# Performance work log

Measured on AMD Instinct MI355X. Metric: run time of the kernel, lower is better.

## Reference

```python
import jax, jax.numpy as jnp
import numpy as np

B, S, D, H = 1, 2048, 1024, 16
DH = D // H  # 64
HID = 4 * D
EPS = 1e-5
NEG = -1.0e9


def setup_inputs() -> dict:
    key = jax.random.key(0)
    ks = jax.random.split(key, 12)
    s = 0.02
    return {
        "y": jax.random.normal(ks[0], (B, S, D), jnp.float32),
        "encoder_output": jax.random.normal(ks[1], (B, S, D), jnp.float32),
        # per-head shared projection (query_fc used for q,k,v — faithful to source bug)
        "Wq_self": jax.random.normal(ks[2], (H, D, DH), jnp.float32) * s,
        "bq_self": jax.random.normal(ks[3], (H, DH), jnp.float32) * s,
        "Wq_cross": jax.random.normal(ks[4], (H, D, DH), jnp.float32) * s,
        "bq_cross": jax.random.normal(ks[5], (H, DH), jnp.float32) * s,
        "g1": jnp.ones((D,), jnp.float32), "beta1": jnp.zeros((D,), jnp.float32),
        "g2": jnp.ones((D,), jnp.float32), "beta2": jnp.zeros((D,), jnp.float32),
        "g3": jnp.ones((D,), jnp.float32), "beta3": jnp.zeros((D,), jnp.float32),
        "w1": jax.random.normal(ks[6], (D, HID), jnp.float32) * s,
        "b1": jax.random.normal(ks[7], (HID,), jnp.float32) * s,
        "w2": jax.random.normal(ks[8], (HID, D), jnp.float32) * s,
        "b2": jax.random.normal(ks[9], (D,), jnp.float32) * s,
    }


def _layernorm(x, g, b):
    mu = jnp.mean(x, axis=-1, keepdims=True)
    var = jnp.mean((x - mu) ** 2, axis=-1, keepdims=True)
    return (x - mu) * jax.lax.rsqrt(var + EPS) * g + b


def _mha(x_q, x_kv, W, bias, causal):
    # source bug: q, k, v all use query_fc projection
    q = jnp.einsum('bsd,hde->bhse', x_q, W) + bias[None, :, None, :]
    k = jnp.einsum('bsd,hde->bhse', x_kv, W) + bias[None, :, None, :]
    v = jnp.einsum('bsd,hde->bhse', x_kv, W) + bias[None, :, None, :]
    scores = jnp.einsum('bhse,bhte->bhst', q, k) / jnp.sqrt(jnp.float32(DH))
    if causal:
        sq, sk = scores.shape[-2], scores.shape[-1]
        mask = jnp.triu(jnp.ones((sq, sk), bool), k=1)
        scores = jnp.where(mask, NEG, scores)
    p = jax.nn.softmax(scores, axis=-1)
    out = jnp.einsum('bhst,bhte->bhse', p, v)  # [B,H,S,DH]
    b, h, s, e = out.shape
    return out.transpose(0, 2, 1, 3).reshape(b, s, h * e)


def reference(y, encoder_output, Wq_self, bq_self, Wq_cross, bq_cross,
              g1, beta1, g2, beta2, g3, beta3, w1, b1, w2, b2):
    sa = _mha(y, y, Wq_self, bq_self, causal=True)
    y1 = _layernorm(y + sa, g1, beta1)
    ca = _mha(y1, encoder_output, Wq_cross, bq_cross, causal=False)
    y2 = _layernorm(y1 + ca, g2, beta2)
    ff = jnp.maximum(y2 @ w1 + b1, 0.0) @ w2 + b2
    return _layernorm(y2 + ff, g3, beta3)
```

## Files before the change

kernel.cpp:

```cpp
#include <hip/hip_runtime.h>
#include <hip/hip_bf16.h>


#define S_LEN 2048
#define DMODEL 1024
#define NHEAD 16
#define DHEAD 64
#define HIDDEN 4096

using bf16 = __hip_bfloat16;
typedef __attribute__((ext_vector_type(8))) short bf16x8;
typedef __attribute__((ext_vector_type(4))) float floatx4;

__device__ __forceinline__ void async_ld16(const void* g, void* l) {
  __builtin_amdgcn_global_load_lds(
      (const __attribute__((address_space(1))) unsigned int*)g,
      (__attribute__((address_space(3))) unsigned int*)l, 16, 0, 0);
}

__device__ __forceinline__ unsigned short f2bf_bits(float f) {
  __hip_bfloat16 b = __float2bfloat16(f);
  return *(unsigned short*)&b;
}

template <bool HEADB>
__global__ __launch_bounds__(256) void transp_bf16_kernel(
    const float* __restrict__ src0, bf16* __restrict__ dst0,
    const float* __restrict__ src1, bf16* __restrict__ dst1, int K, int N) {
  const float* src = blockIdx.z ? src1 : src0;
  bf16* dst = blockIdx.z ? dst1 : dst0;
  __shared__ float tile[32][33];
  const int tx = threadIdx.x & 31, ty = threadIdx.x >> 5;
  const int k0 = blockIdx.y * 32, n0 = blockIdx.x * 32;
#pragma unroll
  for (int i = 0; i < 4; ++i) {
    const int k = k0 + ty + i * 8;
    const int n = n0 + tx;
    size_t idx;
    if (HEADB)
      idx = (size_t)(n >> 6) * ((size_t)K * 64) + (size_t)k * 64 + (n & 63);
    else
      idx = (size_t)k * N + n;
    tile[ty + i * 8][tx] = src[idx];
  }
  __syncthreads();
#pragma unroll
  for (int i = 0; i < 4; ++i) {
    const int n = n0 + ty + i * 8;
    const int k = k0 + tx;
    dst[(size_t)n * K + k] = __float2bfloat16(tile[tx][ty + i * 8]);
  }
}

__global__ __launch_bounds__(256) void conv_bf16_kernel(
    const float* __restrict__ src0, bf16* __restrict__ dst0,
    const float* __restrict__ src1, bf16* __restrict__ dst1, int n4) {
  const float* src = blockIdx.z ? src1 : src0;
  bf16* dst = blockIdx.z ? dst1 : dst0;
  const int i = blockIdx.x * 256 + threadIdx.x;
  if (i >= n4) return;
  float4 v = ((const float4*)src)[i];
  unsigned short r[4] = {f2bf_bits(v.x), f2bf_bits(v.y), f2bf_bits(v.z), f2bf_bits(v.w)};
  ((ushort2*)dst)[i * 2] = make_ushort2(r[0], r[1]);
  ((ushort2*)dst)[i * 2 + 1] = make_ushort2(r[2], r[3]);
}

template <int BM, int BN, bool RELU, bool DUALT, typename CT>
__global__ __launch_bounds__(256) void mfma_gemm_kernel(
    const bf16* __restrict__ A0, const bf16* __restrict__ Bt0,
    const float* __restrict__ bias0, CT* __restrict__ C0,
    bf16* __restrict__ Ct0,
    const bf16* __restrict__ A1, const bf16* __restrict__ Bt1,
    const float* __restrict__ bias1, CT* __restrict__ C1,
    bf16* __restrict__ Ct1,
    int M, int N, int Kstride, int Klen) {
  const bf16* A = blockIdx.z ? A1 : A0;
  const bf16* Bt = blockIdx.z ? Bt1 : Bt0;
  const float* bias = blockIdx.z ? bias1 : bias0;
  CT* C = blockIdx.z ? C1 : C0;
  bf16* Ct = blockIdx.z ? Ct1 : Ct0;

  constexpr int MF = (BM + 31) / 32;
  constexpr int NF = BN / 32;
  __shared__ __align__(16) bf16 As[2][BM * 64];
  __shared__ __align__(16) bf16 Bs[2][BN * 64];

  const int tid = threadIdx.x;
  const int wave = tid >> 6;
  const int lane = tid & 63;
  const int m0 = blockIdx.y * BM;
  const int n0 = blockIdx.x * BN;
  const int wr = wave >> 1, wc = wave & 1;

  const int srow = tid >> 3;
  const int schunk = (tid & 7) ^ (srow & 7);
  const bf16* agp = A + (size_t)(m0 + srow) * Kstride + schunk * 8;
  const bf16* bgp = Bt + (size_t)(n0 + srow) * Kstride + schunk * 8;

  floatx4 acc[MF][NF];
#pragma unroll
  for (int i = 0; i < MF; ++i)
#pragma unroll
    for (int j = 0; j < NF; ++j) acc[i][j] = floatx4{0.f, 0.f, 0.f, 0.f};

  const int mrow = lane & 15;
  const int p0 = (((lane >> 4) ^ (mrow & 7)) << 4);
  const int p1 = p0 ^ 64;

  auto stage = [&](int buf, int kt) {
    char* al = (char*)As + buf * (BM * 128) + wave * 1024;
    char* bl = (char*)Bs + buf * (BN * 128) + wave * 1024;
#pragma unroll
    for (int i = 0; i < BM / 32; ++i)
      async_ld16(agp + (size_t)(32 * i) * Kstride + kt, al + i * 4096);
#pragma unroll
    for (int i = 0; i < BN / 32; ++i)
      async_ld16(bgp + (size_t)(32 * i) * Kstride + kt, bl + i * 4096);
  };

  stage(0, 0);
  __syncthreads();

  int cur = 0;
  for (int kt = 0; kt < Klen; kt += 64) {
    const char* abase = (const char*)As + cur * (BM * 128);
    const char* bbase = (const char*)Bs + cur * (BN * 128);
    bf16x8 af0[MF], af1[MF], bf0[NF], bf1[NF];
#pragma unroll
    for (int fi = 0; fi < MF; ++fi) {
      const char* ar = abase + (wr * (BM / 2) + fi * 16 + mrow) * 128;
      af0[fi] = *(const bf16x8*)(ar + p0);
      af1[fi] = *(const bf16x8*)(ar + p1);
    }
#pragma unroll
    for (int fj = 0; fj < NF; ++fj) {
      const char* br = bbase + (wc * (BN / 2) + fj * 16 + mrow) * 128;
      bf0[fj] = *(const bf16x8*)(br + p0);
      bf1[fj] = *(const bf16x8*)(br + p1);
    }

    if (kt + 64 < Klen) stage(cur ^ 1, kt + 64);

#pragma unroll
    for (int fi = 0; fi < MF; ++fi)
#pragma unroll
      for (int fj = 0; fj < NF; ++fj) {
        acc[fi][fj] = __builtin_amdgcn_mfma_f32_16x16x32_bf16(
            af0[fi], bf0[fj], acc[fi][fj], 0, 0, 0);
        acc[fi][fj] = __builtin_amdgcn_mfma_f32_16x16x32_bf16(
            af1[fi], bf1[fj], acc[fi][fj], 0, 0, 0);
      }

    __syncthreads();
    cur ^= 1;
  }

  const int erow = (lane >> 4) * 4;
  const int ecol = lane & 15;
#pragma unroll
  for (int fi = 0; fi < MF; ++fi) {
#pragma unroll
    for (int fj = 0; fj < NF; ++fj) {
      const int nn = n0 + wc * (BN / 2) + fj * 16 + ecol;
      const float bv = bias ? bias[nn] : 0.0f;
      const int mmb = m0 + wr * (BM / 2) + fi * 16 + erow;
      float v[4];
#pragma unroll
      for (int r = 0; r < 4; ++r) {
        v[r] = acc[fi][fj][r] + bv;
        if (RELU) v[r] = fmaxf(v[r], 0.0f);
        if constexpr (sizeof(CT) == 2)
          C[(size_t)(mmb + r) * N + nn] = (CT)__float2bfloat16(v[r]);
        else
          C[(size_t)(mmb + r) * N + nn] = (CT)v[r];
      }
      if (DUALT) {
        ushort4 pk;
        pk.x = f2bf_bits(v[0]);
        pk.y = f2bf_bits(v[1]);
        pk.z = f2bf_bits(v[2]);
        pk.w = f2bf_bits(v[3]);
        *(ushort4*)&Ct[(size_t)nn * M + mmb] = pk;
      }
    }
  }
}

__global__ __launch_bounds__(256) void mfma_attn_kernel(
    const bf16* __restrict__ Q, const bf16* __restrict__ K,
    const bf16* __restrict__ Vt,
    float* __restrict__ OA, float* __restrict__ OB,
    float* __restrict__ LA, float* __restrict__ LB, int causal) {
  __shared__ __align__(16) unsigned short Kt[2][32 * 64];
  __shared__ __align__(16) unsigned short Vs[2][64 * 32];
  __shared__ __align__(16) unsigned short Ps[4][512];

  const int tid = threadIdx.x;
  const int w = tid >> 6, lane = tid & 63;
  const int g = lane >> 4, c = lane & 15;
  const int h = blockIdx.y;
  const int qb = causal ? ((int)gridDim.x - 1 - (int)blockIdx.x)
                        : (int)blockIdx.x;
  const int q0 = qb * 64;
  const int z = blockIdx.z;
  const int qw = q0 + w * 16;
  float* Oz = z ? OB : OA;
  float* Lz = z ? LB : LA;

  const bf16* qrow = Q + (size_t)(qw + c) * DMODEL + h * DHEAD + g * 8;
  const bf16x8 qfa = *(const bf16x8*)qrow;
  const bf16x8 qfb = *(const bf16x8*)(qrow + 32);

  const int srk = tid >> 3;
  const int sck = (tid & 7) ^ (srk & 7);
  const bf16* kgp = K + (size_t)srk * DMODEL + h * DHEAD + sck * 8;
  const int srv = tid >> 2;
  const int scv = (tid & 3) ^ ((srv >> 1) & 3);
  const bf16* vgp = Vt + (size_t)(h * DHEAD + srv) * S_LEN + scv * 8;

  const int kpos0 = ((g ^ (c & 7)) << 4);
  const int kpos1 = kpos0 ^ 64;
  const int vpos = ((g ^ ((c >> 1) & 3)) << 4);
  char* pswave = (char*)Ps + w * 1024;

  floatx4 of[4];
#pragma unroll
  for (int md = 0; md < 4; ++md) of[md] = floatx4{0.f, 0.f, 0.f, 0.f};
  float lpart = 0.f;

  const int nkt = causal ? (q0 / 32 + 2) : (S_LEN / 32);

  auto stage = [&](int buf, int kt) {
    const int t0 = kt * 32;
    async_ld16(kgp + (size_t)t0 * DMODEL, (char*)Kt + buf * 4096 + w * 1024);
    async_ld16(vgp + t0, (char*)Vs + buf * 4096 + w * 1024);
  };

  stage(0, z);
  __syncthreads();

  int cur = 0;
  for (int kt = z; kt < nkt; kt += 2) {
    const int t0 = kt * 32;
    const bool act = !(causal && t0 >= qw + 16);

    bf16x8 kf00, kf01, kf10, kf11, vf0, vf1, vf2, vf3;
    if (act) {
      const char* kbase = (const char*)Kt + cur * 4096;
      const char* vbase = (const char*)Vs + cur * 4096;
      const char* kr0 = kbase + c * 128;
      const char* kr1 = kbase + (16 + c) * 128;
      kf00 = *(const bf16x8*)(kr0 + kpos0);
      kf01 = *(const bf16x8*)(kr0 + kpos1);
      kf10 = *(const bf16x8*)(kr1 + kpos0);
      kf11 = *(const bf16x8*)(kr1 + kpos1);
      vf0 = *(const bf16x8*)(vbase + (c)*64 + vpos);
      vf1 = *(const bf16x8*)(vbase + (16 + c) * 64 + vpos);
      vf2 = *(const bf16x8*)(vbase + (32 + c) * 64 + vpos);
      vf3 = *(const bf16x8*)(vbase + (48 + c) * 64 + vpos);
    }

    if (kt + 2 < nkt) stage(cur ^ 1, kt + 2);

    if (act) {
      const bool diag = causal && (t0 + 32 > qw);
#pragma unroll
      for (int jt = 0; jt < 2; ++jt) {
        floatx4 s = floatx4{0.f, 0.f, 0.f, 0.f};
        __builtin_amdgcn_s_setprio(1);
        s = __builtin_amdgcn_mfma_f32_16x16x32_bf16(jt ? kf10 : kf00, qfa, s, 0, 0, 0);
        s = __builtin_amdgcn_mfma_f32_16x16x32_bf16(jt ? kf11 : kf01, qfb, s, 0, 0, 0);
        __builtin_amdgcn_s_setprio(0);

        ushort4 pk;
        unsigned short* pp = (unsigned short*)&pk;
#pragma unroll
        for (int r = 0; r < 4; ++r) {
          float p = __expf(0.125f * s[r]);
          if (diag && (t0 + 16 * jt + 4 * g + r > qw + c)) p = 0.0f;
          lpart += p;
          pp[r] = f2bf_bits(p);
        }
        const int pb =
            c * 64 + ((((2 * jt + (g >> 1)) ^ ((c >> 1) & 3)) << 4) |
                      ((g & 1) << 3));
        *(ushort4*)(pswave + pb) = pk;
      }

      const bf16x8 pf = *(const bf16x8*)(pswave + c * 64 + vpos);
      __builtin_amdgcn_s_setprio(1);
      of[0] = __builtin_amdgcn_mfma_f32_16x16x32_bf16(vf0, pf, of[0], 0, 0, 0);
      of[1] = __builtin_amdgcn_mfma_f32_16x16x32_bf16(vf1, pf, of[1], 0, 0, 0);
      of[2] = __builtin_amdgcn_mfma_f32_16x16x32_bf16(vf2, pf, of[2], 0, 0, 0);
      of[3] = __builtin_amdgcn_mfma_f32_16x16x32_bf16(vf3, pf, of[3], 0, 0, 0);
      __builtin_amdgcn_s_setprio(0);
    }

    __syncthreads();
    cur ^= 1;
  }

  lpart += __shfl_xor(lpart, 16, 64);
  lpart += __shfl_xor(lpart, 32, 64);
  if (g == 0) Lz[(size_t)h * S_LEN + qw + c] = lpart;
  float* orow = Oz + (size_t)(qw + c) * DMODEL + h * DHEAD;
#pragma unroll
  for (int md = 0; md < 4; ++md) {
    float4 v;
    v.x = of[md][0];
    v.y = of[md][1];
    v.z = of[md][2];
    v.w = of[md][3];
    *(float4*)(orow + md * 16 + 4 * g) = v;
  }
}

template <bool DUAL, bool MERGE, bool SUM2>
__global__ __launch_bounds__(256) void add_ln_kernel(
    const float* __restrict__ X, const float* __restrict__ R,
    const float* __restrict__ R2, const float* __restrict__ bvec,
    const float* __restrict__ La, const float* __restrict__ Lb,
    const float* __restrict__ g, const float* __restrict__ beta,
    float* __restrict__ out, bf16* __restrict__ out2) {
  const int row = blockIdx.x;
  const int tid = threadIdx.x;

  float v[4];
  float s1 = 0.0f, s2 = 0.0f;
#pragma unroll
  for (int i = 0; i < 4; ++i) {
    const int c = tid + i * 256;
    float x = X[(size_t)row * DMODEL + c];
    if (MERGE) {
      const int h = c >> 6;
      const float rl =
          1.0f / (La[(size_t)h * S_LEN + row] + Lb[(size_t)h * S_LEN + row]);
      x += (R[(size_t)row * DMODEL + c] + R2[(size_t)row * DMODEL + c]) * rl;
    } else if (SUM2) {
      x += R[(size_t)row * DMODEL + c] + R2[(size_t)row * DMODEL + c] + bvec[c];
    } else {
      x += R[(size_t)row * DMODEL + c];
    }
    v[i] = x;
    s1 += x;
    s2 += x * x;
  }
#pragma unroll
  for (int off = 32; off; off >>= 1) {
    s1 += __shfl_xor(s1, off, 64);
    s2 += __shfl_xor(s2, off, 64);
  }
  __shared__ float w1s[4], w2s[4];
  const int wid = tid >> 6, lane = tid & 63;
  if (lane == 0) { w1s[wid] = s1; w2s[wid] = s2; }
  __syncthreads();
  s1 = w1s[0] + w1s[1] + w1s[2] + w1s[3];
  s2 = w2s[0] + w2s[1] + w2s[2] + w2s[3];

  const float mu = s1 * (1.0f / DMODEL);
  const float var = s2 * (1.0f / DMODEL) - mu * mu;
  const float rstd = rsqrtf(var + 1e-5f);

#pragma unroll
  for (int i = 0; i < 4; ++i) {
    const int c = tid + i * 256;
    const float r = (v[i] - mu) * rstd * g[c] + beta[c];
    out[(size_t)row * DMODEL + c] = r;
    if (DUAL) out2[(size_t)row * DMODEL + c] = __float2bfloat16(r);
  }
}

extern "C" void kernel_launch(void* const* d_in, const int* in_sizes, int n_in,
                              void* d_out, int out_size, void* d_ws, size_t ws_size,
                              hipStream_t stream) {
  const float* y      = (const float*)d_in[0];
  const float* enc    = (const float*)d_in[1];
  const float* Wself  = (const float*)d_in[2];
  const float* bself  = (const float*)d_in[3];
  const float* Wcross = (const float*)d_in[4];
  const float* bcross = (const float*)d_in[5];
  const float* g1     = (const float*)d_in[6];
  const float* be1    = (const float*)d_in[7];
  const float* g2     = (const float*)d_in[8];
  const float* be2    = (const float*)d_in[9];
  const float* g3     = (const float*)d_in[10];
  const float* be3    = (const float*)d_in[11];
  const float* w1     = (const float*)d_in[12];
  const float* b1     = (const float*)d_in[13];
  const float* w2     = (const float*)d_in[14];
  const float* b2     = (const float*)d_in[15];
  float* out = (float*)d_out;

  char* ws = (char*)d_ws;
  const size_t MB = 1024 * 1024;
  bf16*  ybf   = (bf16*)(ws + 0 * MB);
  bf16*  encbf = (bf16*)(ws + 4 * MB);
  float* PA    = (float*)(ws + 0 * MB);
  float* PB    = (float*)(ws + 8 * MB);
  float* Y1    = (float*)(ws + 16 * MB);
  float* Y2    = (float*)(ws + 24 * MB);
  bf16*  Q12b  = (bf16*)(ws + 32 * MB);
  bf16*  Q1t   = (bf16*)(ws + 36 * MB);
  bf16*  K2b   = (bf16*)(ws + 40 * MB);
  bf16*  K2t   = (bf16*)(ws + 44 * MB);
  bf16*  w1t   = (bf16*)(ws + 48 * MB);
  bf16*  w2t   = (bf16*)(ws + 56 * MB);
  bf16*  Wst   = (bf16*)(ws + 64 * MB);
  bf16*  Wct   = (bf16*)(ws + 66 * MB);
  bf16*  Y1bf  = (bf16*)(ws + 68 * MB);
  bf16*  Y2bf  = (bf16*)(ws + 72 * MB);
  float* La    = (float*)(ws + 76 * MB);
  float* Lb    = (float*)(ws + 76 * MB + 512 * 1024);
  bf16*  FFH   = (bf16*)(ws + 0 * MB);
  float* FFa   = (float*)(ws + 32 * MB);
  float* FFb   = (float*)(ws + 40 * MB);

  const dim3 blk(256);
  const dim3 gT_w(DMODEL / 32, DMODEL / 32, 2);
  const dim3 gT_w1(HIDDEN / 32, DMODEL / 32);
  const dim3 gT_w2(DMODEL / 32, HIDDEN / 32);
  const dim3 gConv(S_LEN * DMODEL / 4 / 256, 1, 2);
  const dim3 gProj2(DMODEL / 64, S_LEN / 64, 2);
  const dim3 gProj(DMODEL / 64, S_LEN / 32);
  const dim3 gFf1(HIDDEN / 64, S_LEN / 64);
  const dim3 gFf2(DMODEL / 64, S_LEN / 64, 2);
  const dim3 gAttn(S_LEN / 64, NHEAD, 2);
  const dim3 gLn(S_LEN);

  transp_bf16_kernel<true><<<gT_w, blk, 0, stream>>>(
      Wself, Wst, Wcross, Wct, DMODEL, DMODEL);
  transp_bf16_kernel<false><<<gT_w1, blk, 0, stream>>>(
      w1, w1t, nullptr, nullptr, DMODEL, HIDDEN);
  transp_bf16_kernel<false><<<gT_w2, blk, 0, stream>>>(
      w2, w2t, nullptr, nullptr, HIDDEN, DMODEL);
  conv_bf16_kernel<<<gConv, blk, 0, stream>>>(
      y, ybf, enc, encbf, S_LEN * DMODEL / 4);

  mfma_gemm_kernel<64, 64, false, true, bf16><<<gProj2, blk, 0, stream>>>(
      ybf, Wst, bself, Q12b, Q1t,
      encbf, Wct, bcross, K2b, K2t, S_LEN, DMODEL, DMODEL, DMODEL);
  mfma_attn_kernel<<<gAttn, blk, 0, stream>>>(
      Q12b, Q12b, Q1t, PA, PB, La, Lb, 1);
  add_ln_kernel<true, true, false><<<gLn, blk, 0, stream>>>(
      y, PA, PB, nullptr, La, Lb, g1, be1, Y1, Y1bf);
  mfma_gemm_kernel<32, 64, false, false, bf16><<<gProj, blk, 0, stream>>>(
      Y1bf, Wct, bcross, Q12b, nullptr,
      nullptr, nullptr, nullptr, nullptr, nullptr, S_LEN, DMODEL, DMODEL, DMODEL);
  mfma_attn_kernel<<<gAttn, blk, 0, stream>>>(
      Q12b, K2b, K2t, PA, PB, La, Lb, 0);
  add_ln_kernel<true, true, false><<<gLn, blk, 0, stream>>>(
      Y1, PA, PB, nullptr, La, Lb, g2, be2, Y2, Y2bf);
  mfma_gemm_kernel<64, 64, true, false, bf16><<<gFf1, blk, 0, stream>>>(
      Y2bf, w1t, b1, FFH, nullptr,
      nullptr, nullptr, nullptr, nullptr, nullptr, S_LEN, HIDDEN, DMODEL, DMODEL);
  mfma_gemm_kernel<64, 64, false, false, float><<<gFf2, blk, 0, stream>>>(
      FFH, w2t, nullptr, FFa, nullptr,
      FFH + HIDDEN / 2, w2t + HIDDEN / 2, nullptr, FFb, nullptr,
      S_LEN, DMODEL, HIDDEN, HIDDEN / 2);
  add_ln_kernel<false, false, true><<<gLn, blk, 0, stream>>>(
      Y2, FFa, FFb, b2, nullptr, nullptr, g3, be3, out, nullptr);
}
```

Measured before the change: 306.6 us.

## Triple-buffer K/V tiles in attention kernel with one barrier per iteration

Result: slower. 314.3 us (+2.5%).

```diff
diff --git a/kernel.cpp b/kernel.cpp
--- a/kernel.cpp
+++ b/kernel.cpp
@@ -191,8 +191,8 @@
     const bf16* __restrict__ Vt,
     float* __restrict__ OA, float* __restrict__ OB,
     float* __restrict__ LA, float* __restrict__ LB, int causal) {
-  __shared__ __align__(16) unsigned short Kt[2][32 * 64];
-  __shared__ __align__(16) unsigned short Vs[2][64 * 32];
+  __shared__ __align__(16) unsigned short Kt[3][32 * 64];
+  __shared__ __align__(16) unsigned short Vs[3][64 * 32];
   __shared__ __align__(16) unsigned short Ps[4][512];
 
   const int tid = threadIdx.x;
@@ -229,40 +229,49 @@
   float lpart = 0.f;
 
   const int nkt = causal ? (q0 / 32 + 2) : (S_LEN / 32);
-
-  auto stage = [&](int buf, int kt) {
+  const int n_it = (nkt - z + 1) >> 1;
+
+  auto stage = [&](int slot, int kt) {
     const int t0 = kt * 32;
-    async_ld16(kgp + (size_t)t0 * DMODEL, (char*)Kt + buf * 4096 + w * 1024);
-    async_ld16(vgp + t0, (char*)Vs + buf * 4096 + w * 1024);
+    async_ld16(kgp + (size_t)t0 * DMODEL, (char*)Kt + slot * 4096 + w * 1024);
+    async_ld16(vgp + t0, (char*)Vs + slot * 4096 + w * 1024);
   };
 
   stage(0, z);
-  __syncthreads();
-
-  int cur = 0;
-  for (int kt = z; kt < nkt; kt += 2) {
+  {
+    int k1 = z + 2;
+    stage(1, k1 > nkt - 1 ? nkt - 1 : k1);
+  }
+
+  int slot = 0;
+  for (int i = 0; i < n_it; ++i) {
+    const int kt = z + 2 * i;
     const int t0 = kt * 32;
+
+    asm volatile("s_waitcnt vmcnt(2)" ::: "memory");
+    __builtin_amdgcn_s_barrier();
+
+    {
+      const int sl2 = slot >= 1 ? slot - 1 : 2;
+      int kp = z + 2 * (i + 2);
+      stage(sl2, kp > nkt - 1 ? nkt - 1 : kp);
+    }
+
     const bool act = !(causal && t0 >= qw + 16);
-
-    bf16x8 kf00, kf01, kf10, kf11, vf0, vf1, vf2, vf3;
     if (act) {
-      const char* kbase = (const char*)Kt + cur * 4096;
-      const char* vbase = (const char*)Vs + cur * 4096;
+      const char* kbase = (const char*)Kt + slot * 4096;
+      const char* vbase = (const char*)Vs + slot * 4096;
       const char* kr0 = kbase + c * 128;
       const char* kr1 = kbase + (16 + c) * 128;
-      kf00 = *(const bf16x8*)(kr0 + kpos0);
-      kf01 = *(const bf16x8*)(kr0 + kpos1);
-      kf10 = *(const bf16x8*)(kr1 + kpos0);
-      kf11 = *(const bf16x8*)(kr1 + kpos1);
-      vf0 = *(const bf16x8*)(vbase + (c)*64 + vpos);
-      vf1 = *(const bf16x8*)(vbase + (16 + c) * 64 + vpos);
-      vf2 = *(const bf16x8*)(vbase + (32 + c) * 64 + vpos);
-      vf3 = *(const bf16x8*)(vbase + (48 + c) * 64 + vpos);
-    }
-
-    if (kt + 2 < nkt) stage(cur ^ 1, kt + 2);
-
-    if (act) {
+      const bf16x8 kf00 = *(const bf16x8*)(kr0 + kpos0);
+      const bf16x8 kf01 = *(const bf16x8*)(kr0 + kpos1);
+      const bf16x8 kf10 = *(const bf16x8*)(kr1 + kpos0);
+      const bf16x8 kf11 = *(const bf16x8*)(kr1 + kpos1);
+      const bf16x8 vf0 = *(const bf16x8*)(vbase + (c)*64 + vpos);
+      const bf16x8 vf1 = *(const bf16x8*)(vbase + (16 + c) * 64 + vpos);
+      const bf16x8 vf2 = *(const bf16x8*)(vbase + (32 + c) * 64 + vpos);
+      const bf16x8 vf3 = *(const bf16x8*)(vbase + (48 + c) * 64 + vpos);
+
       const bool diag = causal && (t0 + 32 > qw);
 #pragma unroll
       for (int jt = 0; jt < 2; ++jt) {
@@ -296,9 +305,10 @@
       __builtin_amdgcn_s_setprio(0);
     }
 
-    __syncthreads();
-    cur ^= 1;
-  }
+    slot = slot == 2 ? 0 : slot + 1;
+  }
+
+  asm volatile("s_waitcnt vmcnt(0)" ::: "memory");
 
   lpart += __shfl_xor(lpart, 16, 64);
   lpart += __shfl_xor(lpart, 32, 64);
```

## Load attention K/V fragments directly from global into registers, drop LDS staging

Applied to the files above, without the earlier changes.

Measured after the change: 435.9 us. +42.1%, slower.

```diff
diff --git a/kernel.cpp b/kernel.cpp
--- a/kernel.cpp
+++ b/kernel.cpp
@@ -186,21 +186,19 @@
   }
 }
 
-__global__ __launch_bounds__(256) void mfma_attn_kernel(
+__global__ __launch_bounds__(256, 4) void mfma_attn_kernel(
     const bf16* __restrict__ Q, const bf16* __restrict__ K,
     const bf16* __restrict__ Vt,
     float* __restrict__ OA, float* __restrict__ OB,
     float* __restrict__ LA, float* __restrict__ LB, int causal) {
-  __shared__ __align__(16) unsigned short Kt[2][32 * 64];
-  __shared__ __align__(16) unsigned short Vs[2][64 * 32];
   __shared__ __align__(16) unsigned short Ps[4][512];
 
   const int tid = threadIdx.x;
   const int w = tid >> 6, lane = tid & 63;
   const int g = lane >> 4, c = lane & 15;
-  const int h = blockIdx.y;
-  const int qb = causal ? ((int)gridDim.x - 1 - (int)blockIdx.x)
-                        : (int)blockIdx.x;
+  const int h = blockIdx.x;
+  const int qb = causal ? ((int)gridDim.y - 1 - (int)blockIdx.y)
+                        : (int)blockIdx.y;
   const int q0 = qb * 64;
   const int z = blockIdx.z;
   const int qw = q0 + w * 16;
@@ -211,15 +209,9 @@
   const bf16x8 qfa = *(const bf16x8*)qrow;
   const bf16x8 qfb = *(const bf16x8*)(qrow + 32);
 
-  const int srk = tid >> 3;
-  const int sck = (tid & 7) ^ (srk & 7);
-  const bf16* kgp = K + (size_t)srk * DMODEL + h * DHEAD + sck * 8;
-  const int srv = tid >> 2;
-  const int scv = (tid & 3) ^ ((srv >> 1) & 3);
-  const bf16* vgp = Vt + (size_t)(h * DHEAD + srv) * S_LEN + scv * 8;
-
-  const int kpos0 = ((g ^ (c & 7)) << 4);
-  const int kpos1 = kpos0 ^ 64;
+  const bf16* kbase = K + (size_t)c * DMODEL + h * DHEAD + g * 8;
+  const bf16* vbase = Vt + (size_t)(h * DHEAD + c) * S_LEN + g * 8;
+
   const int vpos = ((g ^ ((c >> 1) & 3)) << 4);
   char* pswave = (char*)Ps + w * 1024;
 
@@ -228,76 +220,67 @@
   for (int md = 0; md < 4; ++md) of[md] = floatx4{0.f, 0.f, 0.f, 0.f};
   float lpart = 0.f;
 
-  const int nkt = causal ? (q0 / 32 + 2) : (S_LEN / 32);
-
-  auto stage = [&](int buf, int kt) {
+  const int ktEnd = causal ? ((qw + 47) >> 5) : (S_LEN / 32);
+
+  auto LDALL = [&](bf16x8 (&kk)[4], bf16x8 (&vv)[4], int kt) {
+    const bf16* kp = kbase + (size_t)(kt * 32) * DMODEL;
+    kk[0] = *(const bf16x8*)kp;
+    kk[1] = *(const bf16x8*)(kp + 32);
+    kk[2] = *(const bf16x8*)(kp + 16 * DMODEL);
+    kk[3] = *(const bf16x8*)(kp + 16 * DMODEL + 32);
+    const bf16* vp = vbase + kt * 32;
+    vv[0] = *(const bf16x8*)vp;
+    vv[1] = *(const bf16x8*)(vp + 16 * S_LEN);
+    vv[2] = *(const bf16x8*)(vp + 32 * S_LEN);
+    vv[3] = *(const bf16x8*)(vp + 48 * S_LEN);
+  };
+
+  auto COMPUTE = [&](const bf16x8 (&kk)[4], const bf16x8 (&vv)[4], int kt) {
     const int t0 = kt * 32;
-    async_ld16(kgp + (size_t)t0 * DMODEL, (char*)Kt + buf * 4096 + w * 1024);
-    async_ld16(vgp + t0, (char*)Vs + buf * 4096 + w * 1024);
+    const bool diag = causal && (t0 + 32 > qw);
+#pragma unroll
+    for (int jt = 0; jt < 2; ++jt) {
+      floatx4 s = floatx4{0.f, 0.f, 0.f, 0.f};
+      __builtin_amdgcn_s_setprio(1);
+      s = __builtin_amdgcn_mfma_f32_16x16x32_bf16(kk[2 * jt], qfa, s, 0, 0, 0);
+      s = __builtin_amdgcn_mfma_f32_16x16x32_bf16(kk[2 * jt + 1], qfb, s, 0, 0, 0);
+      __builtin_amdgcn_s_setprio(0);
+
+      ushort4 pk;
+      unsigned short* pp = (unsigned short*)&pk;
+#pragma unroll
+      for (int r = 0; r < 4; ++r) {
+        float p = __expf(0.125f * s[r]);
+        if (diag && (t0 + 16 * jt + 4 * g + r > qw + c)) p = 0.0f;
+        lpart += p;
+        pp[r] = f2bf_bits(p);
+      }
+      const int pb =
+          c * 64 + ((((2 * jt + (g >> 1)) ^ ((c >> 1) & 3)) << 4) |
+                    ((g & 1) << 3));
+      *(ushort4*)(pswave + pb) = pk;
+    }
+
+    const bf16x8 pf = *(const bf16x8*)(pswave + c * 64 + vpos);
+    __builtin_amdgcn_s_setprio(1);
+    of[0] = __builtin_amdgcn_mfma_f32_16x16x32_bf16(vv[0], pf, of[0], 0, 0, 0);
+    of[1] = __builtin_amdgcn_mfma_f32_16x16x32_bf16(vv[1], pf, of[1], 0, 0, 0);
+    of[2] = __builtin_amdgcn_mfma_f32_16x16x32_bf16(vv[2], pf, of[2], 0, 0, 0);
+    of[3] = __builtin_amdgcn_mfma_f32_16x16x32_bf16(vv[3], pf, of[3], 0, 0, 0);
+    __builtin_amdgcn_s_setprio(0);
   };
 
-  stage(0, z);
-  __syncthreads();
-
-  int cur = 0;
-  for (int kt = z; kt < nkt; kt += 2) {
-    const int t0 = kt * 32;
-    const bool act = !(causal && t0 >= qw + 16);
-
-    bf16x8 kf00, kf01, kf10, kf11, vf0, vf1, vf2, vf3;
-    if (act) {
-      const char* kbase = (const char*)Kt + cur * 4096;
-      const char* vbase = (const char*)Vs + cur * 4096;
-      const char* kr0 = kbase + c * 128;
-      const char* kr1 = kbase + (16 + c) * 128;
-      kf00 = *(const bf16x8*)(kr0 + kpos0);
-      kf01 = *(const bf16x8*)(kr0 + kpos1);
-      kf10 = *(const bf16x8*)(kr1 + kpos0);
-      kf11 = *(const bf16x8*)(kr1 + kpos1);
-      vf0 = *(const bf16x8*)(vbase + (c)*64 + vpos);
-      vf1 = *(const bf16x8*)(vbase + (16 + c) * 64 + vpos);
-      vf2 = *(const bf16x8*)(vbase + (32 + c) * 64 + vpos);
-      vf3 = *(const bf16x8*)(vbase + (48 + c) * 64 + vpos);
-    }
-
-    if (kt + 2 < nkt) stage(cur ^ 1, kt + 2);
-
-    if (act) {
-      const bool diag = causal && (t0 + 32 > qw);
-#pragma unroll
-      for (int jt = 0; jt < 2; ++jt) {
-        floatx4 s = floatx4{0.f, 0.f, 0.f, 0.f};
-        __builtin_amdgcn_s_setprio(1);
-        s = __builtin_amdgcn_mfma_f32_16x16x32_bf16(jt ? kf10 : kf00, qfa, s, 0, 0, 0);
-        s = __builtin_amdgcn_mfma_f32_16x16x32_bf16(jt ? kf11 : kf01, qfb, s, 0, 0, 0);
-        __builtin_amdgcn_s_setprio(0);
-
-        ushort4 pk;
-        unsigned short* pp = (unsigned short*)&pk;
-#pragma unroll
-        for (int r = 0; r < 4; ++r) {
-          float p = __expf(0.125f * s[r]);
-          if (diag && (t0 + 16 * jt + 4 * g + r > qw + c)) p = 0.0f;
-          lpart += p;
-          pp[r] = f2bf_bits(p);
-        }
-        const int pb =
-            c * 64 + ((((2 * jt + (g >> 1)) ^ ((c >> 1) & 3)) << 4) |
-                      ((g & 1) << 3));
-        *(ushort4*)(pswave + pb) = pk;
-      }
-
-      const bf16x8 pf = *(const bf16x8*)(pswave + c * 64 + vpos);
-      __builtin_amdgcn_s_setprio(1);
-      of[0] = __builtin_amdgcn_mfma_f32_16x16x32_bf16(vf0, pf, of[0], 0, 0, 0);
-      of[1] = __builtin_amdgcn_mfma_f32_16x16x32_bf16(vf1, pf, of[1], 0, 0, 0);
-      of[2] = __builtin_amdgcn_mfma_f32_16x16x32_bf16(vf2, pf, of[2], 0, 0, 0);
-      of[3] = __builtin_amdgcn_mfma_f32_16x16x32_bf16(vf3, pf, of[3], 0, 0, 0);
-      __builtin_amdgcn_s_setprio(0);
-    }
-
-    __syncthreads();
-    cur ^= 1;
+  bf16x8 ka[4], va[4], kb[4], vb[4];
+  if (z < ktEnd) LDALL(ka, va, z);
+  if (z + 2 < ktEnd) LDALL(kb, vb, z + 2);
+
+  for (int kt = z; kt < ktEnd; kt += 4) {
+    COMPUTE(ka, va, kt);
+    if (kt + 4 < ktEnd) LDALL(ka, va, kt + 4);
+    if (kt + 2 < ktEnd) {
+      COMPUTE(kb, vb, kt + 2);
+      if (kt + 6 < ktEnd) LDALL(kb, vb, kt + 6);
+    }
   }
 
   lpart += __shfl_xor(lpart, 16, 64);
@@ -424,7 +407,7 @@
   const dim3 gProj(DMODEL / 64, S_LEN / 32);
   const dim3 gFf1(HIDDEN / 64, S_LEN / 64);
   const dim3 gFf2(DMODEL / 64, S_LEN / 64, 2);
-  const dim3 gAttn(S_LEN / 64, NHEAD, 2);
+  const dim3 gAttn(NHEAD, S_LEN / 64, 2);
   const dim3 gLn(S_LEN);
 
   transp_bf16_kernel<true><<<gT_w, blk, 0, stream>>>(
```
